# Kernel optimization log

Hardware: AMD Instinct MI355X
Metric: run time of the kernel (lower is better)

The kernel has to match this reference:

```python
import jax, jax.numpy as jnp
import numpy as np

N_NODES = 100000
N_EDGES = 400000
HIDDEN = 128
HEADS = 8
HEAD_DIM = HIDDEN // HEADS


def _lin_params(key, d_in, d_out):
    kw, kb = jax.random.split(key)
    s = 1.0 / np.sqrt(d_in)
    W = jax.random.uniform(kw, (d_in, d_out), jnp.float32, -s, s)
    b = jax.random.uniform(kb, (d_out,), jnp.float32, -s, s)
    return W, b


def setup_inputs() -> dict:
    key = jax.random.key(0)
    ks = jax.random.split(key, 12)
    inp = {
        "x": jax.random.normal(ks[0], (N_NODES, HIDDEN), jnp.float32),
        "edge_attr": jax.random.normal(ks[1], (N_EDGES, HIDDEN), jnp.float32),
        "edge_index": jax.random.randint(ks[2], (2, N_EDGES), 0, N_NODES, dtype=jnp.int32),
        "batch": jnp.zeros((N_NODES,), jnp.int32),
    }
    names = ["Q", "K", "V", "Ew", "Eb", "Ev", "O", "Eo"]
    for i, nm in enumerate(names):
        W, b = _lin_params(ks[3 + i], HIDDEN, HIDDEN)
        inp[f"W_{nm}"] = W
        inp[f"b_{nm}"] = b
    WA, bA = _lin_params(ks[11], HIDDEN, HEADS)
    inp["W_A"] = WA
    inp["b_A"] = bA
    return inp


def signed_sqrt(x):
    return jnp.sign(x) * jnp.sqrt(jnp.abs(x) + 1e-8)


def reference(x, edge_attr, edge_index, batch,
              W_Q, b_Q, W_K, b_K, W_V, b_V,
              W_Ew, b_Ew, W_Eb, b_Eb, W_Ev, b_Ev,
              W_O, b_O, W_Eo, b_Eo, W_A, b_A):
    n = x.shape[0]
    e = edge_index.shape[1]
    h, hd = HEADS, HEAD_DIM
    src, tgt = edge_index[0], edge_index[1]

    Q = (x @ W_Q + b_Q).reshape(n, h, hd)
    K = (x @ W_K + b_K).reshape(n, h, hd)
    V = (x @ W_V + b_V).reshape(n, h, hd)

    # edge-gathered attention features [E, H, HD]
    attn_feat = Q[src] + K[tgt]
    E_w = (edge_attr @ W_Ew + b_Ew).reshape(e, h, hd)
    E_b = (edge_attr @ W_Eb + b_Eb).reshape(e, h, hd)
    attn_feat = signed_sqrt(attn_feat * E_w) + E_b
    attn_feat = jax.nn.relu(attn_feat)

    # per-head scores [E, H], segment softmax over target node
    scores = attn_feat.reshape(e, h * hd) @ W_A + b_A
    seg_max = jax.ops.segment_max(scores, tgt, num_segments=n)
    ex = jnp.exp(scores - seg_max[tgt])
    seg_sum = jax.ops.segment_sum(ex, tgt, num_segments=n)
    alpha = ex / (seg_sum[tgt] + 1e-16)  # [E, H]

    a = alpha[:, :, None]
    E_v = (edge_attr @ W_Ev + b_Ev).reshape(e, h, hd)
    messages = V[src] * a + E_v * a  # [E, H, HD]

    agg = jax.ops.segment_sum(messages, tgt, num_segments=n).reshape(n, h * hd)
    x_out = agg @ W_O + b_O
    edge_attr_out = attn_feat.reshape(e, h * hd) @ W_Eo + b_Eo
    return x_out, edge_attr_out
```

## Files before the change

kernel.cpp:

```cpp
#include <hip/hip_runtime.h>
#include <hip/hip_bf16.h>

typedef __hip_bfloat16 bf16;

#define N_NODES 100000
#define N_EDGES 400000
#define EO_MIN  100000

#define OUT_E_ELEM ((size_t)N_NODES*128)
#define SCORES_B   ((size_t)N_EDGES*8*4)
#define SEG_B      ((size_t)N_NODES*8*4)
#define AGG_BYTES  ((size_t)N_NODES*128*4)
#define WSW_OFF    (SCORES_B + 2*SEG_B)

#define WT_SZ   16384
#define OFF_WQ  (0*WT_SZ)
#define OFF_WK  (2*WT_SZ)
#define OFF_WEW (4*WT_SZ)
#define OFF_WEB (6*WT_SZ)
#define OFF_WEO (8*WT_SZ)
#define OFF_WV  (10*WT_SZ)
#define OFF_WEV (12*WT_SZ)
#define OFF_WA  (14*WT_SZ)
#define WSW_SHORTS (14*WT_SZ + 2*2048)
#define WSW_BYTES  ((size_t)WSW_SHORTS*2)

using short8 = __attribute__((ext_vector_type(8))) short;
using f32x4  = __attribute__((ext_vector_type(4))) float;

__device__ __forceinline__ float b2f(bf16 v){ return __bfloat162float(v); }
__device__ __forceinline__ bf16  f2b(float v){ return __float2bfloat16(v); }
__device__ __forceinline__ short bits(bf16 v){ short s; __builtin_memcpy(&s, &v, 2); return s; }
__device__ __forceinline__ void split(float v, short& h, short& l){
  bf16 hb = f2b(v);
  h = bits(hb);
  l = bits(f2b(v - b2f(hb)));
}
__device__ __forceinline__ float san(float v){
  return (v == v && fabsf(v) < 1e30f) ? v : 0.f;
}
__device__ __forceinline__ unsigned fmap(float f){
  unsigned u = __float_as_uint(f);
  return (u & 0x80000000u) ? ~u : (u | 0x80000000u);
}
__device__ __forceinline__ float funmap(unsigned u){
  unsigned b = (u & 0x80000000u) ? (u ^ 0x80000000u) : ~u;
  return __uint_as_float(b);
}

__global__ void prep_v16(const float* __restrict__ W_Q, const float* __restrict__ W_K,
                         const float* __restrict__ W_Ew, const float* __restrict__ W_Eb,
                         const float* __restrict__ W_Eo, const float* __restrict__ W_V,
                         const float* __restrict__ W_Ev, const float* __restrict__ W_A,
                         short* __restrict__ wsw)
{
  const int b = blockIdx.x;
  if (b < 896){
    const int mi = b >> 7, n = b & 127;
    const float* W = (mi==0)?W_Q:(mi==1)?W_K:(mi==2)?W_Ew:(mi==3)?W_Eb:(mi==4)?W_Eo:(mi==5)?W_V:W_Ev;
    short* dh = wsw + mi*2*WT_SZ;
    short* dl = dh + WT_SZ;
    for (int k = threadIdx.x; k < 128; k += 128){
      short h, l; split(W[(size_t)k*128 + n], h, l);
      dh[n*128 + k] = h; dl[n*128 + k] = l;
    }
  } else {
    const int n = b - 896;
    short* dh = wsw + OFF_WA;
    short* dl = dh + 2048;
    for (int k = threadIdx.x; k < 128; k += 128){
      float v = (n < 8) ? W_A[(size_t)k*8 + n] : 0.f;
      short h, l; split(v, h, l);
      dh[n*128 + k] = h; dl[n*128 + k] = l;
    }
  }
}

__device__ __forceinline__ void stage_row(const float* __restrict__ src,
                                          short* __restrict__ dh, short* __restrict__ dl){
  const float4 v0 = *reinterpret_cast<const float4*>(src);
  const float4 v1 = *reinterpret_cast<const float4*>(src + 4);
  const float vv[8] = {v0.x, v0.y, v0.z, v0.w, v1.x, v1.y, v1.z, v1.w};
  short8 h, l;
  #pragma unroll
  for (int q = 0; q < 8; ++q){ short hh, ll; split(vv[q], hh, ll); h[q] = hh; l[q] = ll; }
  *reinterpret_cast<short8*>(dh) = h;
  *reinterpret_cast<short8*>(dl) = l;
}

__global__ __launch_bounds__(256) void nodeproj_v16(
    const float* __restrict__ x, const short* __restrict__ wsw,
    const float* __restrict__ b_Q, const float* __restrict__ b_K,
    const float* __restrict__ b_V,
    float* __restrict__ Qn, float* __restrict__ Kn, float* __restrict__ Vn,
    int do_v)
{
  __shared__ __align__(16) short Xh[2][2048], Xl[2][2048];
  const int tid = threadIdx.x;
  const int n0  = blockIdx.x * 32;

  {
    const int r = tid & 15, c = tid >> 4;
    #pragma unroll
    for (int rg = 0; rg < 2; ++rg)
      stage_row(x + (size_t)(n0 + rg*16 + r)*128 + c*8,
                &Xh[rg][(c*16 + r)*8], &Xl[rg][(c*16 + r)*8]);
  }
  __syncthreads();

  const int wv = tid >> 6;
  const int mi = (tid & 63) & 15;
  const int kg = (tid & 63) >> 4;

  f32x4 aQ[2][2], aK[2][2], aV[2][2];
  #pragma unroll
  for (int rg = 0; rg < 2; ++rg)
    #pragma unroll
    for (int t = 0; t < 2; ++t){
      aQ[rg][t] = (f32x4){0,0,0,0}; aK[rg][t] = (f32x4){0,0,0,0}; aV[rg][t] = (f32x4){0,0,0,0};
    }

  #pragma unroll
  for (int ks = 0; ks < 4; ++ks){
    const int ao = ((ks*4 + kg)*16 + mi)*8;
    const int kb = ks*32 + kg*8;
    short8 xh[2], xl[2];
    #pragma unroll
    for (int rg = 0; rg < 2; ++rg){
      xh[rg] = *reinterpret_cast<const short8*>(&Xh[rg][ao]);
      xl[rg] = *reinterpret_cast<const short8*>(&Xl[rg][ao]);
    }
    #pragma unroll
    for (int t = 0; t < 2; ++t){
      const int n = (wv*2 + t)*16 + mi;
      const short8 qh = *reinterpret_cast<const short8*>(&wsw[OFF_WQ + n*128 + kb]);
      const short8 ql = *reinterpret_cast<const short8*>(&wsw[OFF_WQ + WT_SZ + n*128 + kb]);
      const short8 kh = *reinterpret_cast<const short8*>(&wsw[OFF_WK + n*128 + kb]);
      const short8 kl = *reinterpret_cast<const short8*>(&wsw[OFF_WK + WT_SZ + n*128 + kb]);
      const short8 vh = *reinterpret_cast<const short8*>(&wsw[OFF_WV + n*128 + kb]);
      const short8 vl = *reinterpret_cast<const short8*>(&wsw[OFF_WV + WT_SZ + n*128 + kb]);
      #pragma unroll
      for (int rg = 0; rg < 2; ++rg){
        aQ[rg][t] = __builtin_amdgcn_mfma_f32_16x16x32_bf16(xh[rg], qh, aQ[rg][t], 0,0,0);
        aK[rg][t] = __builtin_amdgcn_mfma_f32_16x16x32_bf16(xh[rg], kh, aK[rg][t], 0,0,0);
        aQ[rg][t] = __builtin_amdgcn_mfma_f32_16x16x32_bf16(xl[rg], qh, aQ[rg][t], 0,0,0);
        aK[rg][t] = __builtin_amdgcn_mfma_f32_16x16x32_bf16(xl[rg], kh, aK[rg][t], 0,0,0);
        aQ[rg][t] = __builtin_amdgcn_mfma_f32_16x16x32_bf16(xh[rg], ql, aQ[rg][t], 0,0,0);
        aK[rg][t] = __builtin_amdgcn_mfma_f32_16x16x32_bf16(xh[rg], kl, aK[rg][t], 0,0,0);
        if (do_v){
          aV[rg][t] = __builtin_amdgcn_mfma_f32_16x16x32_bf16(xh[rg], vh, aV[rg][t], 0,0,0);
          aV[rg][t] = __builtin_amdgcn_mfma_f32_16x16x32_bf16(xl[rg], vh, aV[rg][t], 0,0,0);
          aV[rg][t] = __builtin_amdgcn_mfma_f32_16x16x32_bf16(xh[rg], vl, aV[rg][t], 0,0,0);
        }
      }
    }
  }

  #pragma unroll
  for (int rg = 0; rg < 2; ++rg)
    #pragma unroll
    for (int t = 0; t < 2; ++t){
      const int n = (wv*2 + t)*16 + mi;
      const float bq = b_Q[n], bk = b_K[n], bv = b_V[n];
      #pragma unroll
      for (int q = 0; q < 4; ++q){
        const size_t row = n0 + rg*16 + kg*4 + q;
        Qn[row*128 + n] = aQ[rg][t][q] + bq;
        Kn[row*128 + n] = aK[rg][t][q] + bk;
        if (do_v) Vn[row*128 + n] = aV[rg][t][q] + bv;
      }
    }
}

__global__ __launch_bounds__(256) void front_qk_v16(
    const float* __restrict__ ea, const int* __restrict__ eidx,
    const float* __restrict__ Qn, const float* __restrict__ Kn,
    const float* __restrict__ b_Ew, const float* __restrict__ b_Eb,
    const float* __restrict__ b_A,  const float* __restrict__ b_Eo,
    const short* __restrict__ wsw,
    float* __restrict__ scores, unsigned* __restrict__ segmax,
    float* __restrict__ oute, int eo_min, int do_score)
{
  __shared__ __align__(16) short eaAFh[2][2048], eaAFl[2][2048];
  __shared__ float qk[32][128];
  __shared__ int sIdx[32], tIdx[32];

  const int tid = threadIdx.x;
  const int e0  = blockIdx.x * 32;

  if (tid < 32){
    sIdx[tid] = eidx[e0 + tid];
    tIdx[tid] = eidx[N_EDGES + e0 + tid];
  }
  __syncthreads();

  {
    const int r = tid & 15, c = tid >> 4;
    #pragma unroll
    for (int rg = 0; rg < 2; ++rg)
      stage_row(ea + (size_t)(e0 + rg*16 + r)*128 + c*8,
                &eaAFh[rg][(c*16 + r)*8], &eaAFl[rg][(c*16 + r)*8]);
  }
  {
    const int r = tid >> 3, cg = tid & 7;
    const float* qp = Qn + (size_t)sIdx[r]*128 + cg*16;
    const float* kp = Kn + (size_t)tIdx[r]*128 + cg*16;
    #pragma unroll
    for (int p = 0; p < 4; ++p){
      const float4 qv = *reinterpret_cast<const float4*>(qp + p*4);
      const float4 kv = *reinterpret_cast<const float4*>(kp + p*4);
      float4 s; s.x = qv.x+kv.x; s.y = qv.y+kv.y; s.z = qv.z+kv.z; s.w = qv.w+kv.w;
      *reinterpret_cast<float4*>(&qk[r][cg*16 + p*4]) = s;
    }
  }
  __syncthreads();

  const int wv = tid >> 6;
  const int mi = (tid & 63) & 15;
  const int kg = (tid & 63) >> 4;

  f32x4 aw[2][2], ab[2][2];
  #pragma unroll
  for (int rg = 0; rg < 2; ++rg)
    #pragma unroll
    for (int t = 0; t < 2; ++t){ aw[rg][t] = (f32x4){0,0,0,0}; ab[rg][t] = (f32x4){0,0,0,0}; }

  #pragma unroll
  for (int ks = 0; ks < 4; ++ks){
    const int ao = ((ks*4 + kg)*16 + mi)*8;
    const int kb = ks*32 + kg*8;
    short8 eh[2], el_[2];
    #pragma unroll
    for (int rg = 0; rg < 2; ++rg){
      eh[rg]  = *reinterpret_cast<const short8*>(&eaAFh[rg][ao]);
      el_[rg] = *reinterpret_cast<const short8*>(&eaAFl[rg][ao]);
    }
    #pragma unroll
    for (int t = 0; t < 2; ++t){
      const int n = (wv*2 + t)*16 + mi;
      const short8 wh = *reinterpret_cast<const short8*>(&wsw[OFF_WEW + n*128 + kb]);
      const short8 wl = *reinterpret_cast<const short8*>(&wsw[OFF_WEW + WT_SZ + n*128 + kb]);
      const short8 bh = *reinterpret_cast<const short8*>(&wsw[OFF_WEB + n*128 + kb]);
      const short8 bl = *reinterpret_cast<const short8*>(&wsw[OFF_WEB + WT_SZ + n*128 + kb]);
      #pragma unroll
      for (int rg = 0; rg < 2; ++rg){
        aw[rg][t] = __builtin_amdgcn_mfma_f32_16x16x32_bf16(eh[rg], wh, aw[rg][t], 0,0,0);
        ab[rg][t] = __builtin_amdgcn_mfma_f32_16x16x32_bf16(eh[rg], bh, ab[rg][t], 0,0,0);
        aw[rg][t] = __builtin_amdgcn_mfma_f32_16x16x32_bf16(el_[rg], wh, aw[rg][t], 0,0,0);
        ab[rg][t] = __builtin_amdgcn_mfma_f32_16x16x32_bf16(el_[rg], bh, ab[rg][t], 0,0,0);
        aw[rg][t] = __builtin_amdgcn_mfma_f32_16x16x32_bf16(eh[rg], wl, aw[rg][t], 0,0,0);
        ab[rg][t] = __builtin_amdgcn_mfma_f32_16x16x32_bf16(eh[rg], bl, ab[rg][t], 0,0,0);
      }
    }
  }

  short afh[2][2][4], afl[2][2][4];
  #pragma unroll
  for (int rg = 0; rg < 2; ++rg)
    #pragma unroll
    for (int t = 0; t < 2; ++t){
      const int n = (wv*2 + t)*16 + mi;
      const float bw = b_Ew[n], bb = b_Eb[n];
      #pragma unroll
      for (int q = 0; q < 4; ++q){
        const float qkv = qk[rg*16 + kg*4 + q][n];
        const float ew  = aw[rg][t][q] + bw;
        const float eb  = ab[rg][t][q] + bb;
        const float pre = qkv * ew;
        const float ssv = pre > 0.f ?  sqrtf( pre + 1e-8f)
                        : (pre < 0.f ? -sqrtf(-pre + 1e-8f) : 0.f);
        const float af = fmaxf(ssv + eb, 0.f);
        short hh, ll; split(af, hh, ll);
        afh[rg][t][q] = hh; afl[rg][t][q] = ll;
      }
    }
  __syncthreads();

  #pragma unroll
  for (int rg = 0; rg < 2; ++rg)
    #pragma unroll
    for (int t = 0; t < 2; ++t){
      const int c  = (wv*2 + t)*2 + (mi >> 3);
      const int k7 = mi & 7;
      #pragma unroll
      for (int q = 0; q < 4; ++q){
        const int idx = (c*16 + kg*4 + q)*8 + k7;
        eaAFh[rg][idx] = afh[rg][t][q];
        eaAFl[rg][idx] = afl[rg][t][q];
      }
    }
  __syncthreads();

  if (do_score && wv < 2){
    const int rg = wv;
    f32x4 acc = {0,0,0,0};
    #pragma unroll
    for (int ks = 0; ks < 4; ++ks){
      const int kb = ks*32 + kg*8;
      const int ao = ((ks*4 + kg)*16 + mi)*8;
      const short8 ah = *reinterpret_cast<const short8*>(&eaAFh[rg][ao]);
      const short8 al = *reinterpret_cast<const short8*>(&eaAFl[rg][ao]);
      const short8 bh = *reinterpret_cast<const short8*>(&wsw[OFF_WA + mi*128 + kb]);
      const short8 bl = *reinterpret_cast<const short8*>(&wsw[OFF_WA + 2048 + mi*128 + kb]);
      acc = __builtin_amdgcn_mfma_f32_16x16x32_bf16(ah, bh, acc, 0,0,0);
      acc = __builtin_amdgcn_mfma_f32_16x16x32_bf16(al, bh, acc, 0,0,0);
      acc = __builtin_amdgcn_mfma_f32_16x16x32_bf16(ah, bl, acc, 0,0,0);
    }
    if (mi < 8){
      const float ba = b_A[mi];
      #pragma unroll
      for (int q = 0; q < 4; ++q){
        const int er = rg*16 + kg*4 + q;
        const float s = san(acc[q] + ba);
        scores[(size_t)(e0 + er)*8 + mi] = s;
        atomicMax(&segmax[(size_t)tIdx[er]*8 + mi], fmap(s));
      }
    }
  }

  if (e0 >= eo_min){
    #pragma unroll
    for (int rg = 0; rg < 2; ++rg)
      #pragma unroll
      for (int t2 = 0; t2 < 2; ++t2){
        const int n = (wv*2 + t2)*16 + mi;
        f32x4 acc = {0,0,0,0};
        #pragma unroll
        for (int ks = 0; ks < 4; ++ks){
          const int kb = ks*32 + kg*8;
          const int ao = ((ks*4 + kg)*16 + mi)*8;
          const short8 ah = *reinterpret_cast<const short8*>(&eaAFh[rg][ao]);
          const short8 al = *reinterpret_cast<const short8*>(&eaAFl[rg][ao]);
          const short8 bh = *reinterpret_cast<const short8*>(&wsw[OFF_WEO + n*128 + kb]);
          const short8 bl = *reinterpret_cast<const short8*>(&wsw[OFF_WEO + WT_SZ + n*128 + kb]);
          acc = __builtin_amdgcn_mfma_f32_16x16x32_bf16(ah, bh, acc, 0,0,0);
          acc = __builtin_amdgcn_mfma_f32_16x16x32_bf16(al, bh, acc, 0,0,0);
          acc = __builtin_amdgcn_mfma_f32_16x16x32_bf16(ah, bl, acc, 0,0,0);
        }
        const float be = b_Eo[n];
        #pragma unroll
        for (int q = 0; q < 4; ++q)
          oute[(size_t)(e0 + rg*16 + kg*4 + q)*128 + n] = san(acc[q] + be);
      }
  }
}

__global__ __launch_bounds__(256) void seg_sum_v16(const float* __restrict__ scores,
    const int* __restrict__ eidx, const unsigned* __restrict__ segmax,
    float* __restrict__ segsum)
{
  int i = blockIdx.x*256 + threadIdx.x;
  if (i >= N_EDGES*8) return;
  int e = i >> 3, h = i & 7;
  int t = eidx[N_EDGES + e];
  float m = funmap(segmax[(size_t)t*8 + h]);
  atomicAdd(&segsum[(size_t)t*8 + h], expf(scores[i] - m));
}

__global__ __launch_bounds__(256) void messages_mfma_v16(
    const float* __restrict__ ea, const int* __restrict__ eidx,
    const float* __restrict__ Vn, const float* __restrict__ b_Ev,
    const short* __restrict__ wsw,
    const float* __restrict__ scores, const unsigned* __restrict__ segmax,
    const float* __restrict__ segsum, float* __restrict__ agg)
{
  __shared__ __align__(16) short Eh[2][2048], El[2][2048];
  __shared__ int sIdx[32], tIdx[32];

  const int tid = threadIdx.x;
  const int e0  = blockIdx.x * 32;

  if (tid < 32){
    sIdx[tid] = eidx[e0 + tid];
    tIdx[tid] = eidx[N_EDGES + e0 + tid];
  }
  __syncthreads();

  {
    const int r = tid & 15, c = tid >> 4;
    #pragma unroll
    for (int rg = 0; rg < 2; ++rg)
      stage_row(ea + (size_t)(e0 + rg*16 + r)*128 + c*8,
                &Eh[rg][(c*16 + r)*8], &El[rg][(c*16 + r)*8]);
  }
  __syncthreads();

  const int wv = tid >> 6;
  const int mi = (tid & 63) & 15;
  const int kg = (tid & 63) >> 4;

  f32x4 aev[2][2];
  #pragma unroll
  for (int rg = 0; rg < 2; ++rg)
    #pragma unroll
    for (int t = 0; t < 2; ++t) aev[rg][t] = (f32x4){0,0,0,0};

  #pragma unroll
  for (int ks = 0; ks < 4; ++ks){
    const int ao = ((ks*4 + kg)*16 + mi)*8;
    const int kb = ks*32 + kg*8;
    short8 eh[2], el_[2];
    #pragma unroll
    for (int rg = 0; rg < 2; ++rg){
      eh[rg]  = *reinterpret_cast<const short8*>(&Eh[rg][ao]);
      el_[rg] = *reinterpret_cast<const short8*>(&El[rg][ao]);
    }
    #pragma unroll
    for (int t = 0; t < 2; ++t){
      const int n = (wv*2 + t)*16 + mi;
      const short8 bh = *reinterpret_cast<const short8*>(&wsw[OFF_WEV + n*128 + kb]);
      const short8 bl = *reinterpret_cast<const short8*>(&wsw[OFF_WEV + WT_SZ + n*128 + kb]);
      #pragma unroll
      for (int rg = 0; rg < 2; ++rg){
        aev[rg][t] = __builtin_amdgcn_mfma_f32_16x16x32_bf16(eh[rg], bh, aev[rg][t], 0,0,0);
        aev[rg][t] = __builtin_amdgcn_mfma_f32_16x16x32_bf16(el_[rg], bh, aev[rg][t], 0,0,0);
        aev[rg][t] = __builtin_amdgcn_mfma_f32_16x16x32_bf16(eh[rg], bl, aev[rg][t], 0,0,0);
      }
    }
  }

  #pragma unroll
  for (int rg = 0; rg < 2; ++rg)
    #pragma unroll
    for (int t = 0; t < 2; ++t){
      const int n = (wv*2 + t)*16 + mi;
      const int h = n >> 4;
      const float be = b_Ev[n];
      #pragma unroll
      for (int q = 0; q < 4; ++q){
        const int row = rg*16 + kg*4 + q;
        const size_t e = (size_t)e0 + row;
        const int s = sIdx[row], tg = tIdx[row];
        const float m   = funmap(segmax[(size_t)tg*8 + h]);
        const float den = segsum[(size_t)tg*8 + h] + 1e-16f;
        const float a   = expf(scores[e*8 + h] - m) / den;
        const float msg = san((Vn[(size_t)s*128 + n] + aev[rg][t][q] + be) * a);
        atomicAdd(&agg[(size_t)tg*128 + n], msg);
      }
    }
}

__global__ __launch_bounds__(256) void messages_v14f(
    const float* __restrict__ x, const float* __restrict__ ea,
    const int* __restrict__ eidx,
    const float* __restrict__ W_V,  const float* __restrict__ b_V,
    const float* __restrict__ W_Ev, const float* __restrict__ b_Ev,
    const float* __restrict__ scores, const unsigned* __restrict__ segmax,
    const float* __restrict__ segsum, float* __restrict__ agg)
{
  __shared__ float eaT[128][16], xsT[128][16];
  __shared__ int sIdx[16], tIdx[16];

  const int tid = threadIdx.x;
  const int e0  = blockIdx.x * 16;

  if (tid < 16){
    sIdx[tid] = eidx[e0 + tid];
    tIdx[tid] = eidx[N_EDGES + e0 + tid];
  }
  __syncthreads();

  for (int idx = tid; idx < 16*128; idx += 256){
    int r = idx >> 7, k = idx & 127;
    eaT[k][r] = ea[(size_t)(e0 + r)*128 + k];
    xsT[k][r] = x[(size_t)sIdx[r]*128 + k];
  }
  __syncthreads();

  const int j  = tid & 127;
  const int h8 = (tid >> 7) * 8;

  float av[8], ae[8];
  #pragma unroll
  for (int i=0;i<8;i++){ av[i]=0.f; ae[i]=0.f; }

  for (int k=0;k<128;k++){
    const float wv = W_V[(size_t)k*128 + j];
    const float we = W_Ev[(size_t)k*128 + j];
    const float4 s0 = *reinterpret_cast<const float4*>(&xsT[k][h8]);
    const float4 s1 = *reinterpret_cast<const float4*>(&xsT[k][h8+4]);
    const float4 e0v = *reinterpret_cast<const float4*>(&eaT[k][h8]);
    const float4 e1v = *reinterpret_cast<const float4*>(&eaT[k][h8+4]);
    const float sv[8] = {s0.x,s0.y,s0.z,s0.w,s1.x,s1.y,s1.z,s1.w};
    const float ev[8] = {e0v.x,e0v.y,e0v.z,e0v.w,e1v.x,e1v.y,e1v.z,e1v.w};
    #pragma unroll
    for (int i=0;i<8;i++){
      av[i] = fmaf(sv[i], wv, av[i]);
      ae[i] = fmaf(ev[i], we, ae[i]);
    }
  }

  const float bv = b_V[j], be = b_Ev[j];
  const int h = j >> 4;
  #pragma unroll
  for (int i=0;i<8;i++){
    const int el = h8 + i;
    const size_t e = (size_t)e0 + el;
    const int t = tIdx[el];
    const float m   = funmap(segmax[(size_t)t*8 + h]);
    const float den = segsum[(size_t)t*8 + h] + 1e-16f;
    const float a   = expf(scores[e*8 + h] - m) / den;
    const float msg = san(((av[i] + bv) + (ae[i] + be)) * a);
    atomicAdd(&agg[(size_t)t*128 + j], msg);
  }
}

__global__ __launch_bounds__(256) void oproj_v16(const float* __restrict__ agg,
    const float* __restrict__ W, const float* __restrict__ bias,
    float* __restrict__ outx)
{
  __shared__ float AT[128][32];
  const int tid  = threadIdx.x;
  const int base = blockIdx.x * 32;

  for (int idx = tid; idx < 32*128; idx += 256){
    int r = idx >> 7, k = idx & 127;
    AT[k][r] = agg[(size_t)(base + r)*128 + k];
  }
  __syncthreads();

  const int j  = tid & 127;
  const int rb = (tid >> 7) * 16;
  float acc[16];
  #pragma unroll
  for (int i=0;i<16;i++) acc[i] = 0.f;

  for (int k=0;k<128;k++){
    const float w = W[(size_t)k*128 + j];
    const float4 a0 = *reinterpret_cast<const float4*>(&AT[k][rb]);
    const float4 a1 = *reinterpret_cast<const float4*>(&AT[k][rb+4]);
    const float4 a2 = *reinterpret_cast<const float4*>(&AT[k][rb+8]);
    const float4 a3 = *reinterpret_cast<const float4*>(&AT[k][rb+12]);
    const float avv[16] = {a0.x,a0.y,a0.z,a0.w,a1.x,a1.y,a1.z,a1.w,
                           a2.x,a2.y,a2.z,a2.w,a3.x,a3.y,a3.z,a3.w};
    #pragma unroll
    for (int i=0;i<16;i++) acc[i] = fmaf(avv[i], w, acc[i]);
  }

  const float bj = bias[j];
  #pragma unroll
  for (int i=0;i<16;i++)
    outx[(size_t)(base + rb + i)*128 + j] = san(acc[i] + bj);
}

template<bool PREPPED>
__global__ __launch_bounds__(256) void front_v14f(
    const float* __restrict__ x, const float* __restrict__ ea,
    const int* __restrict__ eidx,
    const float* __restrict__ W_Q, const float* __restrict__ b_Q,
    const float* __restrict__ W_K, const float* __restrict__ b_K,
    const float* __restrict__ W_Ew, const float* __restrict__ b_Ew,
    const float* __restrict__ W_Eb, const float* __restrict__ b_Eb,
    const float* __restrict__ b_A,
    const float* __restrict__ W_Eo, const float* __restrict__ b_Eo,
    const short* __restrict__ wsw,
    float* __restrict__ scores, unsigned* __restrict__ segmax,
    float* __restrict__ oute, int eo_min)
{
  __shared__ __align__(16) short AFh[3][2048];
  __shared__ __align__(16) short AFl[3][2048];
  __shared__ int sIdx[16], tIdx[16];

  const int tid = threadIdx.x;
  const int e0  = blockIdx.x * 16;

  if (tid < 16){
    sIdx[tid] = eidx[e0 + tid];
    tIdx[tid] = eidx[N_EDGES + e0 + tid];
  }
  __syncthreads();

  {
    const int r = tid & 15, c = tid >> 4;
    const int off = (c*16 + r)*8;
    stage_row(x  + (size_t)sIdx[r]*128 + c*8, &AFh[0][off], &AFl[0][off]);
    stage_row(x  + (size_t)tIdx[r]*128 + c*8, &AFh[1][off], &AFl[1][off]);
    stage_row(ea + (size_t)(e0 + r)*128 + c*8, &AFh[2][off], &AFl[2][off]);
  }
  __syncthreads();

  const int wv = tid >> 6;
  const int mi = (tid & 63) & 15;
  const int kg = (tid & 63) >> 4;

  f32x4 aq[2], ak[2], aw[2], ab[2];
  #pragma unroll
  for (int t = 0; t < 2; ++t){
    aq[t] = (f32x4){0,0,0,0}; ak[t] = (f32x4){0,0,0,0};
    aw[t] = (f32x4){0,0,0,0}; ab[t] = (f32x4){0,0,0,0};
  }

  #pragma unroll
  for (int ks = 0; ks < 4; ++ks){
    const int ao = ((ks*4 + kg)*16 + mi)*8;
    const short8 xh = *reinterpret_cast<const short8*>(&AFh[0][ao]);
    const short8 xl = *reinterpret_cast<const short8*>(&AFl[0][ao]);
    const short8 th = *reinterpret_cast<const short8*>(&AFh[1][ao]);
    const short8 tl = *reinterpret_cast<const short8*>(&AFl[1][ao]);
    const short8 eh = *reinterpret_cast<const short8*>(&AFh[2][ao]);
    const short8 el = *reinterpret_cast<const short8*>(&AFl[2][ao]);
    const int kb = ks*32 + kg*8;

    #pragma unroll
    for (int t = 0; t < 2; ++t){
      const int n = (wv*2 + t)*16 + mi;
      short8 qh, ql, kh, kl, wh, wl, bh, bl;
      if (PREPPED){
        qh = *reinterpret_cast<const short8*>(&wsw[OFF_WQ  + n*128 + kb]);
        ql = *reinterpret_cast<const short8*>(&wsw[OFF_WQ  + WT_SZ + n*128 + kb]);
        kh = *reinterpret_cast<const short8*>(&wsw[OFF_WK  + n*128 + kb]);
        kl = *reinterpret_cast<const short8*>(&wsw[OFF_WK  + WT_SZ + n*128 + kb]);
        wh = *reinterpret_cast<const short8*>(&wsw[OFF_WEW + n*128 + kb]);
        wl = *reinterpret_cast<const short8*>(&wsw[OFF_WEW + WT_SZ + n*128 + kb]);
        bh = *reinterpret_cast<const short8*>(&wsw[OFF_WEB + n*128 + kb]);
        bl = *reinterpret_cast<const short8*>(&wsw[OFF_WEB + WT_SZ + n*128 + kb]);
      } else {
        #pragma unroll
        for (int q = 0; q < 8; ++q){
          short h, l;
          split(W_Q [(size_t)(kb + q)*128 + n], h, l); qh[q] = h; ql[q] = l;
          split(W_K [(size_t)(kb + q)*128 + n], h, l); kh[q] = h; kl[q] = l;
          split(W_Ew[(size_t)(kb + q)*128 + n], h, l); wh[q] = h; wl[q] = l;
          split(W_Eb[(size_t)(kb + q)*128 + n], h, l); bh[q] = h; bl[q] = l;
        }
      }
      aq[t] = __builtin_amdgcn_mfma_f32_16x16x32_bf16(xh, qh, aq[t], 0,0,0);
      ak[t] = __builtin_amdgcn_mfma_f32_16x16x32_bf16(th, kh, ak[t], 0,0,0);
      aw[t] = __builtin_amdgcn_mfma_f32_16x16x32_bf16(eh, wh, aw[t], 0,0,0);
      ab[t] = __builtin_amdgcn_mfma_f32_16x16x32_bf16(eh, bh, ab[t], 0,0,0);
      aq[t] = __builtin_amdgcn_mfma_f32_16x16x32_bf16(xl, qh, aq[t], 0,0,0);
      ak[t] = __builtin_amdgcn_mfma_f32_16x16x32_bf16(tl, kh, ak[t], 0,0,0);
      aw[t] = __builtin_amdgcn_mfma_f32_16x16x32_bf16(el, wh, aw[t], 0,0,0);
      ab[t] = __builtin_amdgcn_mfma_f32_16x16x32_bf16(el, bh, ab[t], 0,0,0);
      aq[t] = __builtin_amdgcn_mfma_f32_16x16x32_bf16(xh, ql, aq[t], 0,0,0);
      ak[t] = __builtin_amdgcn_mfma_f32_16x16x32_bf16(th, kl, ak[t], 0,0,0);
      aw[t] = __builtin_amdgcn_mfma_f32_16x16x32_bf16(eh, wl, aw[t], 0,0,0);
      ab[t] = __builtin_amdgcn_mfma_f32_16x16x32_bf16(eh, bl, ab[t], 0,0,0);
    }
  }

  short afh[2][4], afl[2][4];
  #pragma unroll
  for (int t = 0; t < 2; ++t){
    const int n = (wv*2 + t)*16 + mi;
    const float bqk = b_Q[n] + b_K[n];
    const float bw  = b_Ew[n];
    const float bb  = b_Eb[n];
    #pragma unroll
    for (int q = 0; q < 4; ++q){
      const float qk = aq[t][q] + ak[t][q] + bqk;
      const float ew = aw[t][q] + bw;
      const float eb = ab[t][q] + bb;
      const float pre = qk * ew;
      const float ssv = pre > 0.f ?  sqrtf( pre + 1e-8f)
                      : (pre < 0.f ? -sqrtf(-pre + 1e-8f) : 0.f);
      const float af = fmaxf(ssv + eb, 0.f);
      short hh, ll; split(af, hh, ll);
      afh[t][q] = hh; afl[t][q] = ll;
    }
  }
  __syncthreads();

  #pragma unroll
  for (int t = 0; t < 2; ++t){
    const int c  = (wv*2 + t)*2 + (mi >> 3);
    const int k7 = mi & 7;
    #pragma unroll
    for (int q = 0; q < 4; ++q){
      const int idx = (c*16 + kg*4 + q)*8 + k7;
      AFh[0][idx] = afh[t][q];
      AFl[0][idx] = afl[t][q];
    }
  }
  __syncthreads();

  if (PREPPED && wv == 0){
    f32x4 acc = {0,0,0,0};
    #pragma unroll
    for (int ks = 0; ks < 4; ++ks){
      const int kb = ks*32 + kg*8;
      const int ao = ((ks*4 + kg)*16 + mi)*8;
      const short8 ah = *reinterpret_cast<const short8*>(&AFh[0][ao]);
      const short8 al = *reinterpret_cast<const short8*>(&AFl[0][ao]);
      const short8 bh = *reinterpret_cast<const short8*>(&wsw[OFF_WA + mi*128 + kb]);
      const short8 bl = *reinterpret_cast<const short8*>(&wsw[OFF_WA + 2048 + mi*128 + kb]);
      acc = __builtin_amdgcn_mfma_f32_16x16x32_bf16(ah, bh, acc, 0,0,0);
      acc = __builtin_amdgcn_mfma_f32_16x16x32_bf16(al, bh, acc, 0,0,0);
      acc = __builtin_amdgcn_mfma_f32_16x16x32_bf16(ah, bl, acc, 0,0,0);
    }
    if (mi < 8){
      const float ba = b_A[mi];
      #pragma unroll
      for (int q = 0; q < 4; ++q){
        const int er = kg*4 + q;
        const float s = san(acc[q] + ba);
        scores[(size_t)(e0 + er)*8 + mi] = s;
        atomicMax(&segmax[(size_t)tIdx[er]*8 + mi], fmap(s));
      }
    }
  }

  if (e0 >= eo_min){
    #pragma unroll
    for (int t2 = 0; t2 < 2; ++t2){
      const int n = (wv*2 + t2)*16 + mi;
      f32x4 acc = {0,0,0,0};
      #pragma unroll
      for (int ks = 0; ks < 4; ++ks){
        const int kb = ks*32 + kg*8;
        const int ao = ((ks*4 + kg)*16 + mi)*8;
        const short8 ah = *reinterpret_cast<const short8*>(&AFh[0][ao]);
        const short8 al = *reinterpret_cast<const short8*>(&AFl[0][ao]);
        short8 bh, bl;
        if (PREPPED){
          bh = *reinterpret_cast<const short8*>(&wsw[OFF_WEO + n*128 + kb]);
          bl = *reinterpret_cast<const short8*>(&wsw[OFF_WEO + WT_SZ + n*128 + kb]);
        } else {
          #pragma unroll
          for (int q = 0; q < 8; ++q){
            short h, l; split(W_Eo[(size_t)(kb + q)*128 + n], h, l); bh[q] = h; bl[q] = l;
          }
        }
        acc = __builtin_amdgcn_mfma_f32_16x16x32_bf16(ah, bh, acc, 0,0,0);
        acc = __builtin_amdgcn_mfma_f32_16x16x32_bf16(al, bh, acc, 0,0,0);
        acc = __builtin_amdgcn_mfma_f32_16x16x32_bf16(ah, bl, acc, 0,0,0);
      }
      const float be = b_Eo[n];
      #pragma unroll
      for (int q = 0; q < 4; ++q)
        oute[(size_t)(e0 + kg*4 + q)*128 + n] = san(acc[q] + be);
    }
  }
}

extern "C" void kernel_launch(void* const* d_in, const int* in_sizes, int n_in,
                              void* d_out, int out_size, void* d_ws, size_t ws_size,
                              hipStream_t stream)
{
  (void)in_sizes; (void)n_in; (void)out_size;
  const float* x    = (const float*)d_in[0];
  const float* ea   = (const float*)d_in[1];
  const int*   eidx = (const int*)d_in[2];
  const float* W_Q  = (const float*)d_in[4];  const float* b_Q  = (const float*)d_in[5];
  const float* W_K  = (const float*)d_in[6];  const float* b_K  = (const float*)d_in[7];
  const float* W_V  = (const float*)d_in[8];  const float* b_V  = (const float*)d_in[9];
  const float* W_Ew = (const float*)d_in[10]; const float* b_Ew = (const float*)d_in[11];
  const float* W_Eb = (const float*)d_in[12]; const float* b_Eb = (const float*)d_in[13];
  const float* W_Ev = (const float*)d_in[14]; const float* b_Ev = (const float*)d_in[15];
  const float* W_O  = (const float*)d_in[16]; const float* b_O  = (const float*)d_in[17];
  const float* W_Eo = (const float*)d_in[18]; const float* b_Eo = (const float*)d_in[19];
  const float* W_A  = (const float*)d_in[20]; const float* b_A  = (const float*)d_in[21];

  float* out_x = (float*)d_out;
  float* oute  = out_x + OUT_E_ELEM;

  float*    scores = (float*)d_out;
  unsigned* segmax = (unsigned*)((char*)d_out + SCORES_B);
  float*    segsum = (float*)((char*)d_out + SCORES_B + SEG_B);

  const size_t SZ_NODEF = (size_t)N_NODES*128*4;
  const size_t NEED_QK   = 2*SZ_NODEF + WSW_BYTES;
  const size_t NEED_FULL = 3*SZ_NODEF + WSW_BYTES;

  const int tier = (ws_size >= NEED_FULL) ? 2 : (ws_size >= NEED_QK) ? 1 : 0;

  dim3 blk(256);
  hipMemsetAsync((void*)segmax, 0, 2*SEG_B, stream);

  if (tier >= 1){
    char*  ws  = (char*)d_ws;
    float* Qn  = (float*)ws;
    float* Kn  = (float*)(ws + SZ_NODEF);
    float* Vn  = (tier == 2) ? (float*)(ws + 2*SZ_NODEF) : nullptr;
    short* wsw = (short*)(ws + ((tier == 2) ? 3 : 2)*SZ_NODEF);
    float* agg = Qn;

    prep_v16<<<dim3(912), dim3(128), 0, stream>>>(W_Q, W_K, W_Ew, W_Eb, W_Eo, W_V, W_Ev, W_A, wsw);

    nodeproj_v16<<<dim3(N_NODES/32), blk, 0, stream>>>(x, wsw, b_Q, b_K, b_V,
        Qn, Kn, Vn, tier == 2 ? 1 : 0);

    front_qk_v16<<<dim3(N_EDGES/32), blk, 0, stream>>>(ea, eidx, Qn, Kn,
        b_Ew, b_Eb, b_A, b_Eo, wsw, scores, segmax, oute, 0, 1);

    hipMemsetAsync((void*)agg, 0, AGG_BYTES, stream);

    seg_sum_v16<<<dim3((N_EDGES*8 + 255)/256), blk, 0, stream>>>(scores, eidx, segmax, segsum);

    if (tier == 2)
      messages_mfma_v16<<<dim3(N_EDGES/32), blk, 0, stream>>>(ea, eidx, Vn, b_Ev,
          wsw, scores, segmax, segsum, agg);
    else
      messages_v14f<<<dim3(N_EDGES/16), blk, 0, stream>>>(x, ea, eidx,
          W_V, b_V, W_Ev, b_Ev, scores, segmax, segsum, agg);

    oproj_v16<<<dim3(N_NODES/32), blk, 0, stream>>>(agg, W_O, b_O, out_x);

  } else {
    short* wsw = (short*)((char*)d_out + WSW_OFF);
    float* agg = oute;

    hipMemsetAsync((void*)agg, 0, AGG_BYTES, stream);

    prep_v16<<<dim3(912), dim3(128), 0, stream>>>(W_Q, W_K, W_Ew, W_Eb, W_Eo, W_V, W_Ev, W_A, wsw);

    front_v14f<true><<<dim3(N_EDGES/16), blk, 0, stream>>>(x, ea, eidx,
        W_Q, b_Q, W_K, b_K, W_Ew, b_Ew, W_Eb, b_Eb, b_A, W_Eo, b_Eo, wsw,
        scores, segmax, oute, EO_MIN);

    seg_sum_v16<<<dim3((N_EDGES*8 + 255)/256), blk, 0, stream>>>(scores, eidx, segmax, segsum);

    messages_v14f<<<dim3(N_EDGES/16), blk, 0, stream>>>(x, ea, eidx,
        W_V, b_V, W_Ev, b_Ev, scores, segmax, segsum, agg);

    oproj_v16<<<dim3(N_NODES/32), blk, 0, stream>>>(agg, W_O, b_O, out_x);

    front_v14f<false><<<dim3(EO_MIN/16), blk, 0, stream>>>(x, ea, eidx,
        W_Q, b_Q, W_K, b_K, W_Ew, b_Ew, W_Eb, b_Eb, b_A, W_Eo, b_Eo, nullptr,
        nullptr, nullptr, oute, 0);
  }
}
```

Baseline: 972.1 us.

## Fold softmax denominator into message pass and defer normalization to output projection

In the workspace path, the separate seg_sum kernel is removed. The message kernel now accumulates unnormalized exp-weighted messages and atomically sums the denominators per target and head. The output projection divides by the denominator when it loads agg. front_qk also shares one shared-memory buffer between the edge-attribute staging and the Q+K gather, and the Q/K gather now happens after the first MFMA stage, which cuts LDS use and may raise occupancy. The cost is one extra atomic per head per edge and a memset that also clears the denominator buffer, which aliases Kn.

```diff
diff --git a/kernel.cpp b/kernel.cpp
--- a/kernel.cpp
+++ b/kernel.cpp
@@ -48,7 +48,7 @@
   return __uint_as_float(b);
 }
 
-__global__ void prep_v16(const float* __restrict__ W_Q, const float* __restrict__ W_K,
+__global__ void prep_v18(const float* __restrict__ W_Q, const float* __restrict__ W_K,
                          const float* __restrict__ W_Ew, const float* __restrict__ W_Eb,
                          const float* __restrict__ W_Eo, const float* __restrict__ W_V,
                          const float* __restrict__ W_Ev, const float* __restrict__ W_A,
@@ -88,7 +88,7 @@
   *reinterpret_cast<short8*>(dl) = l;
 }
 
-__global__ __launch_bounds__(256) void nodeproj_v16(
+__global__ __launch_bounds__(256) void nodeproj_v18(
     const float* __restrict__ x, const short* __restrict__ wsw,
     const float* __restrict__ b_Q, const float* __restrict__ b_K,
     const float* __restrict__ b_V,
@@ -172,18 +172,20 @@
     }
 }
 
-__global__ __launch_bounds__(256) void front_qk_v16(
+__global__ __launch_bounds__(256) void front_qk_v18(
     const float* __restrict__ ea, const int* __restrict__ eidx,
     const float* __restrict__ Qn, const float* __restrict__ Kn,
     const float* __restrict__ b_Ew, const float* __restrict__ b_Eb,
     const float* __restrict__ b_A,  const float* __restrict__ b_Eo,
     const short* __restrict__ wsw,
     float* __restrict__ scores, unsigned* __restrict__ segmax,
-    float* __restrict__ oute, int eo_min, int do_score)
+    float* __restrict__ oute, int do_score)
 {
-  __shared__ __align__(16) short eaAFh[2][2048], eaAFl[2][2048];
-  __shared__ float qk[32][128];
+  __shared__ __align__(16) char smem[16384];
   __shared__ int sIdx[32], tIdx[32];
+  short* AFh = (short*)smem;
+  short* AFl = (short*)(smem + 8192);
+  float* qkf = (float*)smem;
 
   const int tid = threadIdx.x;
   const int e0  = blockIdx.x * 32;
@@ -192,26 +194,12 @@
     sIdx[tid] = eidx[e0 + tid];
     tIdx[tid] = eidx[N_EDGES + e0 + tid];
   }
-  __syncthreads();
-
   {
     const int r = tid & 15, c = tid >> 4;
     #pragma unroll
     for (int rg = 0; rg < 2; ++rg)
       stage_row(ea + (size_t)(e0 + rg*16 + r)*128 + c*8,
-                &eaAFh[rg][(c*16 + r)*8], &eaAFl[rg][(c*16 + r)*8]);
-  }
-  {
-    const int r = tid >> 3, cg = tid & 7;
-    const float* qp = Qn + (size_t)sIdx[r]*128 + cg*16;
-    const float* kp = Kn + (size_t)tIdx[r]*128 + cg*16;
-    #pragma unroll
-    for (int p = 0; p < 4; ++p){
-      const float4 qv = *reinterpret_cast<const float4*>(qp + p*4);
-      const float4 kv = *reinterpret_cast<const float4*>(kp + p*4);
-      float4 s; s.x = qv.x+kv.x; s.y = qv.y+kv.y; s.z = qv.z+kv.z; s.w = qv.w+kv.w;
-      *reinterpret_cast<float4*>(&qk[r][cg*16 + p*4]) = s;
-    }
+                &AFh[rg*2048 + (c*16 + r)*8], &AFl[rg*2048 + (c*16 + r)*8]);
   }
   __syncthreads();
 
@@ -232,8 +220,8 @@
     short8 eh[2], el_[2];
     #pragma unroll
     for (int rg = 0; rg < 2; ++rg){
-      eh[rg]  = *reinterpret_cast<const short8*>(&eaAFh[rg][ao]);
-      el_[rg] = *reinterpret_cast<const short8*>(&eaAFl[rg][ao]);
+      eh[rg]  = *reinterpret_cast<const short8*>(&AFh[rg*2048 + ao]);
+      el_[rg] = *reinterpret_cast<const short8*>(&AFl[rg*2048 + ao]);
     }
     #pragma unroll
     for (int t = 0; t < 2; ++t){
@@ -253,6 +241,21 @@
       }
     }
   }
+  __syncthreads();
+
+  {
+    const int r = tid >> 3, cg = tid & 7;
+    const float* qp = Qn + (size_t)sIdx[r]*128 + cg*16;
+    const float* kp = Kn + (size_t)tIdx[r]*128 + cg*16;
+    #pragma unroll
+    for (int p = 0; p < 4; ++p){
+      const float4 qv = *reinterpret_cast<const float4*>(qp + p*4);
+      const float4 kv = *reinterpret_cast<const float4*>(kp + p*4);
+      float4 s; s.x = qv.x+kv.x; s.y = qv.y+kv.y; s.z = qv.z+kv.z; s.w = qv.w+kv.w;
+      *reinterpret_cast<float4*>(&qkf[r*128 + cg*16 + p*4]) = s;
+    }
+  }
+  __syncthreads();
 
   short afh[2][2][4], afl[2][2][4];
   #pragma unroll
@@ -263,7 +266,7 @@
       const float bw = b_Ew[n], bb = b_Eb[n];
       #pragma unroll
       for (int q = 0; q < 4; ++q){
-        const float qkv = qk[rg*16 + kg*4 + q][n];
+        const float qkv = qkf[(rg*16 + kg*4 + q)*128 + n];
         const float ew  = aw[rg][t][q] + bw;
         const float eb  = ab[rg][t][q] + bb;
         const float pre = qkv * ew;
@@ -285,8 +288,8 @@
       #pragma unroll
       for (int q = 0; q < 4; ++q){
         const int idx = (c*16 + kg*4 + q)*8 + k7;
-        eaAFh[rg][idx] = afh[rg][t][q];
-        eaAFl[rg][idx] = afl[rg][t][q];
+        AFh[rg*2048 + idx] = afh[rg][t][q];
+        AFl[rg*2048 + idx] = afl[rg][t][q];
       }
     }
   __syncthreads();
@@ -298,8 +301,8 @@
     for (int ks = 0; ks < 4; ++ks){
       const int kb = ks*32 + kg*8;
       const int ao = ((ks*4 + kg)*16 + mi)*8;
-      const short8 ah = *reinterpret_cast<const short8*>(&eaAFh[rg][ao]);
-      const short8 al = *reinterpret_cast<const short8*>(&eaAFl[rg][ao]);
+      const short8 ah = *reinterpret_cast<const short8*>(&AFh[rg*2048 + ao]);
+      const short8 al = *reinterpret_cast<const short8*>(&AFl[rg*2048 + ao]);
       const short8 bh = *reinterpret_cast<const short8*>(&wsw[OFF_WA + mi*128 + kb]);
       const short8 bl = *reinterpret_cast<const short8*>(&wsw[OFF_WA + 2048 + mi*128 + kb]);
       acc = __builtin_amdgcn_mfma_f32_16x16x32_bf16(ah, bh, acc, 0,0,0);
@@ -318,34 +321,32 @@
     }
   }
 
-  if (e0 >= eo_min){
-    #pragma unroll
-    for (int rg = 0; rg < 2; ++rg)
-      #pragma unroll
-      for (int t2 = 0; t2 < 2; ++t2){
-        const int n = (wv*2 + t2)*16 + mi;
-        f32x4 acc = {0,0,0,0};
-        #pragma unroll
-        for (int ks = 0; ks < 4; ++ks){
-          const int kb = ks*32 + kg*8;
-          const int ao = ((ks*4 + kg)*16 + mi)*8;
-          const short8 ah = *reinterpret_cast<const short8*>(&eaAFh[rg][ao]);
-          const short8 al = *reinterpret_cast<const short8*>(&eaAFl[rg][ao]);
-          const short8 bh = *reinterpret_cast<const short8*>(&wsw[OFF_WEO + n*128 + kb]);
-          const short8 bl = *reinterpret_cast<const short8*>(&wsw[OFF_WEO + WT_SZ + n*128 + kb]);
-          acc = __builtin_amdgcn_mfma_f32_16x16x32_bf16(ah, bh, acc, 0,0,0);
-          acc = __builtin_amdgcn_mfma_f32_16x16x32_bf16(al, bh, acc, 0,0,0);
-          acc = __builtin_amdgcn_mfma_f32_16x16x32_bf16(ah, bl, acc, 0,0,0);
-        }
-        const float be = b_Eo[n];
-        #pragma unroll
-        for (int q = 0; q < 4; ++q)
-          oute[(size_t)(e0 + rg*16 + kg*4 + q)*128 + n] = san(acc[q] + be);
-      }
-  }
-}
-
-__global__ __launch_bounds__(256) void seg_sum_v16(const float* __restrict__ scores,
+  #pragma unroll
+  for (int rg = 0; rg < 2; ++rg)
+    #pragma unroll
+    for (int t2 = 0; t2 < 2; ++t2){
+      const int n = (wv*2 + t2)*16 + mi;
+      f32x4 acc = {0,0,0,0};
+      #pragma unroll
+      for (int ks = 0; ks < 4; ++ks){
+        const int kb = ks*32 + kg*8;
+        const int ao = ((ks*4 + kg)*16 + mi)*8;
+        const short8 ah = *reinterpret_cast<const short8*>(&AFh[rg*2048 + ao]);
+        const short8 al = *reinterpret_cast<const short8*>(&AFl[rg*2048 + ao]);
+        const short8 bh = *reinterpret_cast<const short8*>(&wsw[OFF_WEO + n*128 + kb]);
+        const short8 bl = *reinterpret_cast<const short8*>(&wsw[OFF_WEO + WT_SZ + n*128 + kb]);
+        acc = __builtin_amdgcn_mfma_f32_16x16x32_bf16(ah, bh, acc, 0,0,0);
+        acc = __builtin_amdgcn_mfma_f32_16x16x32_bf16(al, bh, acc, 0,0,0);
+        acc = __builtin_amdgcn_mfma_f32_16x16x32_bf16(ah, bl, acc, 0,0,0);
+      }
+      const float be = b_Eo[n];
+      #pragma unroll
+      for (int q = 0; q < 4; ++q)
+        oute[(size_t)(e0 + rg*16 + kg*4 + q)*128 + n] = san(acc[q] + be);
+    }
+}
+
+__global__ __launch_bounds__(256) void seg_sum_v18(const float* __restrict__ scores,
     const int* __restrict__ eidx, const unsigned* __restrict__ segmax,
     float* __restrict__ segsum)
 {
@@ -357,12 +358,12 @@
   atomicAdd(&segsum[(size_t)t*8 + h], expf(scores[i] - m));
 }
 
-__global__ __launch_bounds__(256) void messages_mfma_v16(
+__global__ __launch_bounds__(256) void messages_mfma_v18(
     const float* __restrict__ ea, const int* __restrict__ eidx,
     const float* __restrict__ Vn, const float* __restrict__ b_Ev,
     const short* __restrict__ wsw,
     const float* __restrict__ scores, const unsigned* __restrict__ segmax,
-    const float* __restrict__ segsum, float* __restrict__ agg)
+    float* __restrict__ den, float* __restrict__ agg)
 {
   __shared__ __align__(16) short Eh[2][2048], El[2][2048];
   __shared__ int sIdx[32], tIdx[32];
@@ -374,8 +375,6 @@
     sIdx[tid] = eidx[e0 + tid];
     tIdx[tid] = eidx[N_EDGES + e0 + tid];
   }
-  __syncthreads();
-
   {
     const int r = tid & 15, c = tid >> 4;
     #pragma unroll
@@ -431,11 +430,11 @@
         const int row = rg*16 + kg*4 + q;
         const size_t e = (size_t)e0 + row;
         const int s = sIdx[row], tg = tIdx[row];
-        const float m   = funmap(segmax[(size_t)tg*8 + h]);
-        const float den = segsum[(size_t)tg*8 + h] + 1e-16f;
-        const float a   = expf(scores[e*8 + h] - m) / den;
-        const float msg = san((Vn[(size_t)s*128 + n] + aev[rg][t][q] + be) * a);
+        const float m    = funmap(segmax[(size_t)tg*8 + h]);
+        const float expw = expf(scores[e*8 + h] - m);
+        const float msg  = san((Vn[(size_t)s*128 + n] + aev[rg][t][q] + be) * expw);
         atomicAdd(&agg[(size_t)tg*128 + n], msg);
+        if (mi == 0) atomicAdd(&den[(size_t)tg*8 + h], expw);
       }
     }
 }
@@ -498,14 +497,15 @@
     const size_t e = (size_t)e0 + el;
     const int t = tIdx[el];
     const float m   = funmap(segmax[(size_t)t*8 + h]);
-    const float den = segsum[(size_t)t*8 + h] + 1e-16f;
-    const float a   = expf(scores[e*8 + h] - m) / den;
+    const float d   = segsum[(size_t)t*8 + h] + 1e-16f;
+    const float a   = expf(scores[e*8 + h] - m) / d;
     const float msg = san(((av[i] + bv) + (ae[i] + be)) * a);
     atomicAdd(&agg[(size_t)t*128 + j], msg);
   }
 }
 
-__global__ __launch_bounds__(256) void oproj_v16(const float* __restrict__ agg,
+__global__ __launch_bounds__(256) void oproj_v18(const float* __restrict__ agg,
+    const float* __restrict__ den,
     const float* __restrict__ W, const float* __restrict__ bias,
     float* __restrict__ outx)
 {
@@ -515,7 +515,9 @@
 
   for (int idx = tid; idx < 32*128; idx += 256){
     int r = idx >> 7, k = idx & 127;
-    AT[k][r] = agg[(size_t)(base + r)*128 + k];
+    float v = agg[(size_t)(base + r)*128 + k];
+    if (den) v /= (den[(size_t)(base + r)*8 + (k >> 4)] + 1e-16f);
+    AT[k][r] = v;
   }
   __syncthreads();
 
@@ -774,27 +776,28 @@
     float* Vn  = (tier == 2) ? (float*)(ws + 2*SZ_NODEF) : nullptr;
     short* wsw = (short*)(ws + ((tier == 2) ? 3 : 2)*SZ_NODEF);
     float* agg = Qn;
-
-    prep_v16<<<dim3(912), dim3(128), 0, stream>>>(W_Q, W_K, W_Ew, W_Eb, W_Eo, W_V, W_Ev, W_A, wsw);
-
-    nodeproj_v16<<<dim3(N_NODES/32), blk, 0, stream>>>(x, wsw, b_Q, b_K, b_V,
+    float* den = Kn;
+
+    prep_v18<<<dim3(912), dim3(128), 0, stream>>>(W_Q, W_K, W_Ew, W_Eb, W_Eo, W_V, W_Ev, W_A, wsw);
+
+    nodeproj_v18<<<dim3(N_NODES/32), blk, 0, stream>>>(x, wsw, b_Q, b_K, b_V,
         Qn, Kn, Vn, tier == 2 ? 1 : 0);
 
-    front_qk_v16<<<dim3(N_EDGES/32), blk, 0, stream>>>(ea, eidx, Qn, Kn,
-        b_Ew, b_Eb, b_A, b_Eo, wsw, scores, segmax, oute, 0, 1);
-
-    hipMemsetAsync((void*)agg, 0, AGG_BYTES, stream);
-
-    seg_sum_v16<<<dim3((N_EDGES*8 + 255)/256), blk, 0, stream>>>(scores, eidx, segmax, segsum);
-
-    if (tier == 2)
-      messages_mfma_v16<<<dim3(N_EDGES/32), blk, 0, stream>>>(ea, eidx, Vn, b_Ev,
-          wsw, scores, segmax, segsum, agg);
-    else
+    front_qk_v18<<<dim3(N_EDGES/32), blk, 0, stream>>>(ea, eidx, Qn, Kn,
+        b_Ew, b_Eb, b_A, b_Eo, wsw, scores, segmax, oute, 1);
+
+    hipMemsetAsync((void*)agg, 0, AGG_BYTES + SEG_B, stream);
+
+    if (tier == 2){
+      messages_mfma_v18<<<dim3(N_EDGES/32), blk, 0, stream>>>(ea, eidx, Vn, b_Ev,
+          wsw, scores, segmax, den, agg);
+      oproj_v18<<<dim3(N_NODES/32), blk, 0, stream>>>(agg, den, W_O, b_O, out_x);
+    } else {
+      seg_sum_v18<<<dim3((N_EDGES*8 + 255)/256), blk, 0, stream>>>(scores, eidx, segmax, segsum);
       messages_v14f<<<dim3(N_EDGES/16), blk, 0, stream>>>(x, ea, eidx,
           W_V, b_V, W_Ev, b_Ev, scores, segmax, segsum, agg);
-
-    oproj_v16<<<dim3(N_NODES/32), blk, 0, stream>>>(agg, W_O, b_O, out_x);
+      oproj_v18<<<dim3(N_NODES/32), blk, 0, stream>>>(agg, nullptr, W_O, b_O, out_x);
+    }
 
   } else {
     short* wsw = (short*)((char*)d_out + WSW_OFF);
@@ -802,18 +805,18 @@
 
     hipMemsetAsync((void*)agg, 0, AGG_BYTES, stream);
 
-    prep_v16<<<dim3(912), dim3(128), 0, stream>>>(W_Q, W_K, W_Ew, W_Eb, W_Eo, W_V, W_Ev, W_A, wsw);
+    prep_v18<<<dim3(912), dim3(128), 0, stream>>>(W_Q, W_K, W_Ew, W_Eb, W_Eo, W_V, W_Ev, W_A, wsw);
 
     front_v14f<true><<<dim3(N_EDGES/16), blk, 0, stream>>>(x, ea, eidx,
         W_Q, b_Q, W_K, b_K, W_Ew, b_Ew, W_Eb, b_Eb, b_A, W_Eo, b_Eo, wsw,
         scores, segmax, oute, EO_MIN);
 
-    seg_sum_v16<<<dim3((N_EDGES*8 + 255)/256), blk, 0, stream>>>(scores, eidx, segmax, segsum);
+    seg_sum_v18<<<dim3((N_EDGES*8 + 255)/256), blk, 0, stream>>>(scores, eidx, segmax, segsum);
 
     messages_v14f<<<dim3(N_EDGES/16), blk, 0, stream>>>(x, ea, eidx,
         W_V, b_V, W_Ev, b_Ev, scores, segmax, segsum, agg);
 
-    oproj_v16<<<dim3(N_NODES/32), blk, 0, stream>>>(agg, W_O, b_O, out_x);
+    oproj_v18<<<dim3(N_NODES/32), blk, 0, stream>>>(agg, nullptr, W_O, b_O, out_x);
 
     front_v14f<false><<<dim3(EO_MIN/16), blk, 0, stream>>>(x, ea, eidx,
         W_Q, b_Q, W_K, b_K, W_Ew, b_Ew, W_Eb, b_Eb, b_A, W_Eo, b_Eo, nullptr,
```

Result: slower. 1.037 ms (+6.7%).
